# Kernel optimization log

Measured on AMD Instinct MI355X. Metric: run time of the kernel, lower is better.

Reference implementation:

```python
import math
import jax, jax.numpy as jnp
import numpy as np

H = 16          # n_heads
WIN = 512       # window_size (causal, one-sided)
BS = 64         # block_size


def setup_inputs() -> dict:
    key = jax.random.key(0)
    ks = jax.random.split(key, 5)
    B, T, D = 2, 4096, 1024
    x = jax.random.normal(ks[0], (B, T, D), dtype=jnp.float32)
    init = 0.02
    Wq = jax.random.normal(ks[1], (D, D), dtype=jnp.float32) * init
    Wk = jax.random.normal(ks[2], (D, D), dtype=jnp.float32) * init
    Wv = jax.random.normal(ks[3], (D, D), dtype=jnp.float32) * init
    Wo = jax.random.normal(ks[4], (D, D), dtype=jnp.float32) * init
    return {"x": x, "Wq": Wq, "Wk": Wk, "Wv": Wv, "Wo": Wo}


def _sliding_window_attn(q, k, v):
    """Causal sliding-window attention, banded/block-sparse form.

    q,k,v: (B, H, T, hd). Only key blocks within the window of each query
    block are gathered, honoring the sparsity the torch mask encodes.
    """
    B, Hn, T, hd = q.shape
    nb = T // BS                   # number of blocks
    nw1 = WIN // BS + 1            # key blocks touching a query block
    scale = 1.0 / math.sqrt(hd)

    qb = q.reshape(B, Hn, nb, BS, hd)
    kb = k.reshape(B, Hn, nb, BS, hd)
    vb = v.reshape(B, Hn, nb, BS, hd)

    offs = jnp.arange(-(WIN // BS), 1)                 # (nw1,)
    idx_raw = jnp.arange(nb)[:, None] + offs[None, :]  # (nb, nw1)
    idx = jnp.clip(idx_raw, 0, nb - 1)

    kg = jnp.take(kb, idx, axis=2)   # (B,H,nb,nw1,BS,hd)
    vg = jnp.take(vb, idx, axis=2)

    scores = jnp.einsum('bhnqd,bhnwkd->bhnqwk', qb, kg) * scale

    qpos = (jnp.arange(nb) * BS)[:, None, None, None] + jnp.arange(BS)[None, :, None, None]  # (nb,BS,1,1)
    kpos = (idx_raw * BS)[:, None, :, None] + jnp.arange(BS)[None, None, None, :]            # (nb,1,nw1,BS)
    valid = (idx_raw[:, None, :, None] >= 0) & (kpos <= qpos) & (qpos - kpos < WIN)
    scores = jnp.where(valid[None, None], scores, -1e9)

    p = jax.nn.softmax(scores.reshape(B, Hn, nb, BS, nw1 * BS), axis=-1)
    p = p.reshape(B, Hn, nb, BS, nw1, BS)
    out = jnp.einsum('bhnqwk,bhnwkd->bhnqd', p, vg)
    return out.reshape(B, Hn, T, hd)


def reference(x, Wq, Wk, Wv, Wo):
    B, T, D = x.shape
    hd = D // H

    def proj(W):  # torch Linear: x @ W.T
        return (x @ W.T).reshape(B, T, H, hd).transpose(0, 2, 1, 3)

    q, k, v = proj(Wq), proj(Wk), proj(Wv)
    out = _sliding_window_attn(q, k, v)            # (B,H,T,hd)
    out = out.transpose(0, 2, 1, 3).reshape(B, T, D)
    return out @ Wo.T
```

## Files before the change

kernel.cpp:

```cpp
#include <hip/hip_runtime.h>

#define DI static __device__ __forceinline__

typedef __attribute__((ext_vector_type(8))) short short8;
typedef __attribute__((ext_vector_type(4))) float f32x4;

DI unsigned short f2bf(float f) {
    union { float f; unsigned int u; } v; v.f = f;
    unsigned int r = v.u + 0x7FFFu + ((v.u >> 16) & 1u);
    return (unsigned short)(r >> 16);
}

DI void gload_lds16(const void* g, void* l) {
    __builtin_amdgcn_global_load_lds(
        (const __attribute__((address_space(1))) void*)g,
        (__attribute__((address_space(3))) void*)l, 16, 0, 0);
}

DI short8 ldsfrag(const void* base, int row, int bytecol) {
    return *(const short8*)((const char*)base + row * 128 + (bytecol ^ ((row & 7) << 4)));
}

__global__ __launch_bounds__(256) void k_cvt(
    const float* __restrict__ x, const float* __restrict__ wq,
    const float* __restrict__ wk, const float* __restrict__ wv,
    const float* __restrict__ wo,
    unsigned short* __restrict__ xb, unsigned short* __restrict__ wqb,
    unsigned short* __restrict__ wkb, unsigned short* __restrict__ wvb,
    unsigned short* __restrict__ wob)
{
    int idx = (blockIdx.x * 256 + threadIdx.x) * 4;
    const float* src; unsigned short* dst; int off;
    if (idx < 8388608) {
        src = x; dst = xb; off = idx;
    } else {
        int rel = idx - 8388608;
        int sel = rel >> 20;
        off = rel & 1048575;
        switch (sel) {
            case 0:  src = wq; dst = wqb; break;
            case 1:  src = wk; dst = wkb; break;
            case 2:  src = wv; dst = wvb; break;
            default: src = wo; dst = wob; break;
        }
    }
    float4 v = *(const float4*)(src + off);
    unsigned long long o = (unsigned long long)f2bf(v.x)
        | ((unsigned long long)f2bf(v.y) << 16)
        | ((unsigned long long)f2bf(v.z) << 32)
        | ((unsigned long long)f2bf(v.w) << 48);
    *(unsigned long long*)(dst + off) = o;
}

DI void gemm_core(const unsigned short* __restrict__ Ag,
                  const unsigned short* __restrict__ Bg,
                  int m0, int n0, char* smem, f32x4 acc[4][4])
{
    const int t = threadIdx.x, lane = t & 63;
    const int wid = t >> 6, wr = wid >> 2, wc = wid & 3;
    const int kl = lane & 15, hi = lane >> 4;

#pragma unroll
    for (int m = 0; m < 4; ++m)
#pragma unroll
        for (int n = 0; n < 4; ++n)
            acc[m][n] = f32x4{0.f, 0.f, 0.f, 0.f};

    const int ca  = t,       ra  = ca  >> 2, sa  = ((ca  & 3) ^ ((ra  >> 1) & 3)) * 8;
    const int cb0 = t,       rb0 = cb0 >> 2, sb0 = ((cb0 & 3) ^ ((rb0 >> 1) & 3)) * 8;
    const int cb1 = t + 512, rb1 = cb1 >> 2, sb1 = ((cb1 & 3) ^ ((rb1 >> 1) & 3)) * 8;
    const unsigned short* pa  = Ag + (long)(m0 + ra)  * 1024 + sa;
    const unsigned short* pb0 = Bg + (long)(n0 + rb0) * 1024 + sb0;
    const unsigned short* pb1 = Bg + (long)(n0 + rb1) * 1024 + sb1;

#define STAGE(TILE, BUF) do {                                          \
        char* _sb = smem + (BUF) * 24576;                              \
        gload_lds16(pa  + (TILE) * 32, _sb + ca * 16);                 \
        gload_lds16(pb0 + (TILE) * 32, _sb + 8192 + cb0 * 16);         \
        gload_lds16(pb1 + (TILE) * 32, _sb + 8192 + cb1 * 16);         \
    } while (0)

    STAGE(0, 0);
    STAGE(1, 1);

    const int swz = ((hi ^ ((kl >> 1) & 3)) << 4);
    const int aoff = (wr * 64 + kl) * 64 + swz;
    const int boff = 8192 + (wc * 64 + kl) * 64 + swz;

#define KSTEP(KS, CUR, PRE, ISSUE, VM) do {                                   \
        asm volatile("s_waitcnt vmcnt(" VM ")" ::: "memory");                 \
        __builtin_amdgcn_s_barrier();                                         \
        __builtin_amdgcn_sched_barrier(0);                                    \
        if (ISSUE) STAGE((KS) + 2, PRE);                                      \
        const char* _ab = smem + (CUR) * 24576 + aoff;                        \
        const char* _bb = smem + (CUR) * 24576 + boff;                        \
        short8 _fa[4], _fb[4];                                                \
        _Pragma("unroll")                                                     \
        for (int m = 0; m < 4; ++m) _fa[m] = *(const short8*)(_ab + m * 1024);\
        _Pragma("unroll")                                                     \
        for (int n = 0; n < 4; ++n) _fb[n] = *(const short8*)(_bb + n * 1024);\
        __builtin_amdgcn_s_setprio(1);                                        \
        _Pragma("unroll")                                                     \
        for (int m = 0; m < 4; ++m)                                           \
        _Pragma("unroll")                                                     \
            for (int n = 0; n < 4; ++n)                                       \
                acc[m][n] = __builtin_amdgcn_mfma_f32_16x16x32_bf16(          \
                    _fa[m], _fb[n], acc[m][n], 0, 0, 0);                      \
        __builtin_amdgcn_s_setprio(0);                                        \
    } while (0)

    for (int u = 0; u < 10; ++u) {
        const int ks = u * 3;
        KSTEP(ks + 0, 0, 2, 1, "3");
        KSTEP(ks + 1, 1, 0, 1, "3");
        KSTEP(ks + 2, 2, 1, 1, "3");
    }
    KSTEP(30, 0, 2, 0, "3");
    KSTEP(31, 1, 0, 0, "0");
#undef KSTEP
#undef STAGE
}

DI void gemm_core128(const unsigned short* __restrict__ Ag,
                     const unsigned short* __restrict__ Bg,
                     int m0, int n0, char* smem, f32x4 acc[4][4])
{
    const int t = threadIdx.x, lane = t & 63;
    const int wid = t >> 6, wr = wid >> 1, wc = wid & 1;
    const int kl = lane & 15, hi = lane >> 4;

#pragma unroll
    for (int m = 0; m < 4; ++m)
#pragma unroll
        for (int n = 0; n < 4; ++n)
            acc[m][n] = f32x4{0.f, 0.f, 0.f, 0.f};

    const int ca0 = t,       ra0 = ca0 >> 2, sa0 = ((ca0 & 3) ^ ((ra0 >> 1) & 3)) * 8;
    const int ca1 = t + 256, ra1 = ca1 >> 2, sa1 = ((ca1 & 3) ^ ((ra1 >> 1) & 3)) * 8;
    const unsigned short* pa0 = Ag + (long)(m0 + ra0) * 1024 + sa0;
    const unsigned short* pa1 = Ag + (long)(m0 + ra1) * 1024 + sa1;
    const unsigned short* pb0 = Bg + (long)(n0 + ra0) * 1024 + sa0;
    const unsigned short* pb1 = Bg + (long)(n0 + ra1) * 1024 + sa1;

#define STAGE(TILE, BUF) do {                                          \
        char* _sb = smem + (BUF) * 16384;                              \
        gload_lds16(pa0 + (TILE) * 32, _sb + ca0 * 16);                \
        gload_lds16(pa1 + (TILE) * 32, _sb + ca1 * 16);                \
        gload_lds16(pb0 + (TILE) * 32, _sb + 8192 + ca0 * 16);         \
        gload_lds16(pb1 + (TILE) * 32, _sb + 8192 + ca1 * 16);         \
    } while (0)

    STAGE(0, 0);
    STAGE(1, 1);

    const int swz = ((hi ^ ((kl >> 1) & 3)) << 4);
    const int aoff = (wr * 64 + kl) * 64 + swz;
    const int boff = 8192 + (wc * 64 + kl) * 64 + swz;

#define KSTEP(KS, CUR, PRE, ISSUE, VM) do {                                   \
        asm volatile("s_waitcnt vmcnt(" VM ")" ::: "memory");                 \
        __builtin_amdgcn_s_barrier();                                         \
        __builtin_amdgcn_sched_barrier(0);                                    \
        if (ISSUE) STAGE((KS) + 2, PRE);                                      \
        const char* _ab = smem + (CUR) * 16384 + aoff;                        \
        const char* _bb = smem + (CUR) * 16384 + boff;                        \
        short8 _fa[4], _fb[4];                                                \
        _Pragma("unroll")                                                     \
        for (int m = 0; m < 4; ++m) _fa[m] = *(const short8*)(_ab + m * 1024);\
        _Pragma("unroll")                                                     \
        for (int n = 0; n < 4; ++n) _fb[n] = *(const short8*)(_bb + n * 1024);\
        __builtin_amdgcn_s_setprio(1);                                        \
        _Pragma("unroll")                                                     \
        for (int m = 0; m < 4; ++m)                                           \
        _Pragma("unroll")                                                     \
            for (int n = 0; n < 4; ++n)                                       \
                acc[m][n] = __builtin_amdgcn_mfma_f32_16x16x32_bf16(          \
                    _fa[m], _fb[n], acc[m][n], 0, 0, 0);                      \
        __builtin_amdgcn_s_setprio(0);                                        \
    } while (0)

    for (int u = 0; u < 10; ++u) {
        const int ks = u * 3;
        KSTEP(ks + 0, 0, 2, 1, "4");
        KSTEP(ks + 1, 1, 0, 1, "4");
        KSTEP(ks + 2, 2, 1, 1, "4");
    }
    KSTEP(30, 0, 2, 0, "4");
    KSTEP(31, 1, 0, 0, "0");
#undef KSTEP
#undef STAGE
}

__global__ __launch_bounds__(512, 4) void k_gemm_qkv(
    const unsigned short* __restrict__ xb,
    const unsigned short* __restrict__ wqb, const unsigned short* __restrict__ wkb,
    const unsigned short* __restrict__ wvb,
    unsigned short* __restrict__ Qo, unsigned short* __restrict__ Ko,
    unsigned short* __restrict__ VTo)
{
    extern __shared__ char smem[];
    const int bx = blockIdx.x, by = blockIdx.y;
    const int w = by >> 2, nb = by & 3;
    const unsigned short* Bw = (w == 0) ? wqb : ((w == 1) ? wkb : wvb);
    const float sc = (w == 0) ? 0.18033688011112042f : 1.0f;

    f32x4 acc[4][4];
    gemm_core(xb, Bw, bx * 128, nb * 256, smem, acc);

    const int t = threadIdx.x, lane = t & 63, wid = t >> 6;
    const int wr = wid >> 2, wc = wid & 3, kl = lane & 15, hi = lane >> 4;
    const int h = nb * 4 + wc;

    if (w < 2) {
        unsigned short* Ow = (w == 0) ? Qo : Ko;
#pragma unroll
        for (int m = 0; m < 4; ++m)
#pragma unroll
            for (int r = 0; r < 4; ++r) {
                int grow = bx * 128 + wr * 64 + m * 16 + hi * 4 + r;
                int bi = grow >> 12, tt = grow & 4095;
                unsigned short* rowp = Ow + ((long)(bi * 16 + h) * 4096 + tt) * 64;
#pragma unroll
                for (int n = 0; n < 4; ++n)
                    rowp[n * 16 + kl] = f2bf(acc[m][n][r] * sc);
            }
    } else {
#pragma unroll
        for (int m = 0; m < 4; ++m)
#pragma unroll
            for (int r = 0; r < 4; ++r) {
                int grow = bx * 128 + wr * 64 + m * 16 + hi * 4 + r;
                int bi = grow >> 12, tt = grow & 4095;
                unsigned short* hb = VTo + (long)(bi * 16 + h) * 262144;
#pragma unroll
                for (int n = 0; n < 4; ++n) {
                    int d = n * 16 + kl;
                    hb[(long)d * 4096 + tt] = f2bf(acc[m][n][r]);
                }
            }
    }
}

__global__ __launch_bounds__(512) void k_attn(
    const unsigned short* __restrict__ Q, const unsigned short* __restrict__ K,
    const unsigned short* __restrict__ VT, unsigned short* __restrict__ AO)
{
    __shared__ unsigned short Qs[8192];
    __shared__ unsigned short Ks[2][4096], Vs[2][4096];
    const int t = threadIdx.x, lane = t & 63, wid = t >> 6;
    const int kl = lane & 15, hi = lane >> 4;
    const int bid = blockIdx.x;
    const int sid = (bid & 7) * 128 + (bid >> 3);
    const int qi = sid & 31, bh = sid >> 5;
    const int b = bh >> 4, h = bh & 15;
    const int iA = qi * 2, iB = qi * 2 + 1;
    const int myI = (wid < 4) ? iA : iB;
    const char* qg = (const char*)(Q + ((long)bh * 4096 + qi * 128) * 64);
    const char* kg = (const char*)(K + (long)bh * 4096 * 64);
    const char* vg = (const char*)(VT + (long)bh * 64 * 4096);

    const int cq0 = t, cq1 = t + 512;
    const int rq0 = cq0 >> 3, sq0 = ((cq0 & 7) * 16) ^ ((rq0 & 7) << 4);
    const int rq1 = cq1 >> 3, sq1 = ((cq1 & 7) * 16) ^ ((rq1 & 7) << 4);
    const int rk = t >> 3, swk = ((t & 7) * 16) ^ ((rk & 7) << 4);
    const char* kgt = kg + rk * 128 + swk;
    const char* vgt = vg + rk * 8192 + swk;

    const int jlo = (iA >= 8) ? iA - 8 : 0;
    const int jhi = iB;

    gload_lds16(qg + rq0 * 128 + sq0, (char*)Qs + cq0 * 16);
    gload_lds16(qg + rq1 * 128 + sq1, (char*)Qs + cq1 * 16);
    gload_lds16(kgt + jlo * 8192, (char*)Ks[0] + t * 16);
    gload_lds16(vgt + jlo * 128,  (char*)Vs[0] + t * 16);
    __syncthreads();

    short8 aq[2];
    aq[0] = ldsfrag(Qs, wid * 16 + kl, hi * 16);
    aq[1] = ldsfrag(Qs, wid * 16 + kl, 64 + hi * 16);

    float lsum[4] = {0.f, 0.f, 0.f, 0.f};
    f32x4 o[4];
#pragma unroll
    for (int nt = 0; nt < 4; ++nt) o[nt] = f32x4{0.f, 0.f, 0.f, 0.f};

    const int qrow = (wid & 3) * 16 + hi * 4;
    char* pw = (char*)Qs + wid * 2048;

    for (int j = jlo; j <= jhi; ++j) {
        const int buf = (j - jlo) & 1;
        if (j < jhi) {
            const int nb = buf ^ 1;
            gload_lds16(kgt + (j + 1) * 8192, (char*)Ks[nb] + t * 16);
            gload_lds16(vgt + (j + 1) * 128,  (char*)Vs[nb] + t * 16);
        }

        const bool act = (wid < 4) ? (j <= iA) : (j >= iB - 8);
        if (act) {
            f32x4 s[4];
#pragma unroll
            for (int nt = 0; nt < 4; ++nt) {
                s[nt] = f32x4{0.f, 0.f, 0.f, 0.f};
#pragma unroll
                for (int kk = 0; kk < 2; ++kk)
                    s[nt] = __builtin_amdgcn_mfma_f32_16x16x32_bf16(
                        aq[kk], ldsfrag(Ks[buf], nt * 16 + kl, kk * 64 + hi * 16),
                        s[nt], 0, 0, 0);
            }

            if (j == myI) {
#pragma unroll
                for (int nt = 0; nt < 4; ++nt) {
                    int key = nt * 16 + kl;
#pragma unroll
                    for (int r = 0; r < 4; ++r)
                        if (key > qrow + r) s[nt][r] = -1e9f;
                }
            } else if (myI - j == 8) {
#pragma unroll
                for (int nt = 0; nt < 4; ++nt) {
                    int key = nt * 16 + kl;
#pragma unroll
                    for (int r = 0; r < 4; ++r)
                        if (key <= qrow + r) s[nt][r] = -1e9f;
                }
            }

#pragma unroll
            for (int nt = 0; nt < 4; ++nt)
#pragma unroll
                for (int r = 0; r < 4; ++r) {
                    float p = exp2f(s[nt][r]);
                    s[nt][r] = p;
                    lsum[r] += p;
                }

#pragma unroll
            for (int nt = 0; nt < 4; ++nt)
#pragma unroll
                for (int r = 0; r < 4; ++r) {
                    int q = hi * 4 + r;
                    int colb = (nt * 16 + kl) * 2;
                    *(unsigned short*)(pw + q * 128 + (colb ^ ((q & 7) << 4))) =
                        f2bf(s[nt][r]);
                }

            short8 pa0 = ldsfrag(pw, kl, hi * 16);
            short8 pa1 = ldsfrag(pw, kl, 64 + hi * 16);
#pragma unroll
            for (int nt = 0; nt < 4; ++nt) {
                o[nt] = __builtin_amdgcn_mfma_f32_16x16x32_bf16(
                    pa0, ldsfrag(Vs[buf], nt * 16 + kl, hi * 16), o[nt], 0, 0, 0);
                o[nt] = __builtin_amdgcn_mfma_f32_16x16x32_bf16(
                    pa1, ldsfrag(Vs[buf], nt * 16 + kl, 64 + hi * 16), o[nt], 0, 0, 0);
            }
        }

        __syncthreads();
    }

#pragma unroll
    for (int d = 1; d < 16; d <<= 1)
#pragma unroll
        for (int r = 0; r < 4; ++r) lsum[r] += __shfl_xor(lsum[r], d);

    float inv[4];
#pragma unroll
    for (int r = 0; r < 4; ++r) inv[r] = 1.0f / lsum[r];
#pragma unroll
    for (int r = 0; r < 4; ++r) {
        int tt = qi * 128 + wid * 16 + hi * 4 + r;
        unsigned short* rowp = AO + ((long)(b * 4096 + tt)) * 1024 + h * 64;
#pragma unroll
        for (int nt = 0; nt < 4; ++nt)
            rowp[nt * 16 + kl] = f2bf(o[nt][r] * inv[r]);
    }
}

__global__ __launch_bounds__(256, 3) void k_gemm_out(
    const unsigned short* __restrict__ AO, const unsigned short* __restrict__ wob,
    float* __restrict__ out)
{
    extern __shared__ char smem[];
    const int bx = blockIdx.x, nb = blockIdx.y;
    f32x4 acc[4][4];
    gemm_core128(AO, wob, bx * 128, nb * 128, smem, acc);

    const int t = threadIdx.x, lane = t & 63, wid = t >> 6;
    const int wr = wid >> 1, wc = wid & 1, kl = lane & 15, hi = lane >> 4;
#pragma unroll
    for (int m = 0; m < 4; ++m)
#pragma unroll
        for (int r = 0; r < 4; ++r) {
            int grow = bx * 128 + wr * 64 + m * 16 + hi * 4 + r;
            float* rowp = out + (long)grow * 1024 + nb * 128 + wc * 64;
#pragma unroll
            for (int n = 0; n < 4; ++n)
                rowp[n * 16 + kl] = acc[m][n][r];
        }
}

extern "C" void kernel_launch(void* const* d_in, const int* in_sizes, int n_in,
                              void* d_out, int out_size, void* d_ws, size_t ws_size,
                              hipStream_t stream) {
    const float* x  = (const float*)d_in[0];
    const float* wq = (const float*)d_in[1];
    const float* wk = (const float*)d_in[2];
    const float* wv = (const float*)d_in[3];
    const float* wo = (const float*)d_in[4];

    char* ws = (char*)d_ws;
    const size_t MB = 1024 * 1024;
    unsigned short* xb  = (unsigned short*)(ws);
    unsigned short* wqb = (unsigned short*)(ws + 16 * MB);
    unsigned short* wkb = (unsigned short*)(ws + 18 * MB);
    unsigned short* wvb = (unsigned short*)(ws + 20 * MB);
    unsigned short* wob = (unsigned short*)(ws + 22 * MB);
    unsigned short* Qp  = (unsigned short*)(ws + 24 * MB);
    unsigned short* Kp  = (unsigned short*)(ws + 40 * MB);
    unsigned short* VTp = (unsigned short*)(ws + 56 * MB);
    unsigned short* AOp = xb;

    hipFuncSetAttribute((const void*)k_gemm_qkv,
                        hipFuncAttributeMaxDynamicSharedMemorySize, 73728);
    hipFuncSetAttribute((const void*)k_gemm_out,
                        hipFuncAttributeMaxDynamicSharedMemorySize, 49152);

    dim3 blk(256);
    k_cvt<<<12288, blk, 0, stream>>>(x, wq, wk, wv, wo,
                                     xb, wqb, wkb, wvb, wob);
    k_gemm_qkv<<<dim3(64, 12), 512, 73728, stream>>>(xb, wqb, wkb, wvb,
                                                     Qp, Kp, VTp);
    k_attn<<<1024, 512, 0, stream>>>(Qp, Kp, VTp, AOp);
    k_gemm_out<<<dim3(64, 8), 256, 49152, stream>>>(AOp, wob, (float*)d_out);
}
```

Measured before the change: 136.5 us.

## Enlarge QKV GEMM tile to 256x256 with 64-wide K and ping-pong LDS

The QKV projection GEMM now computes a 256x256 output tile per 512-thread block instead of 128x256. Each wave holds an 8x4 accumulator array and works through 64-wide K tiles with two LDS buffers of 64KB each. The MFMA work is split into four phases that interleave LDS fragment reads with compute. This aims for higher arithmetic intensity and fewer global loads per FLOP, but the grid shrinks to 384 blocks, LDS use grows to 128KB, and register pressure rises, which lowers occupancy.

```diff
diff --git a/kernel.cpp b/kernel.cpp
--- a/kernel.cpp
+++ b/kernel.cpp
@@ -52,73 +52,165 @@
     *(unsigned long long*)(dst + off) = o;
 }
 
-DI void gemm_core(const unsigned short* __restrict__ Ag,
-                  const unsigned short* __restrict__ Bg,
-                  int m0, int n0, char* smem, f32x4 acc[4][4])
+DI void gemm8p(const unsigned short* __restrict__ Ag,
+               const unsigned short* __restrict__ Bg,
+               int m0, int n0, char* smem, f32x4 acc[8][4])
 {
     const int t = threadIdx.x, lane = t & 63;
     const int wid = t >> 6, wr = wid >> 2, wc = wid & 3;
     const int kl = lane & 15, hi = lane >> 4;
 
 #pragma unroll
-    for (int m = 0; m < 4; ++m)
+    for (int m = 0; m < 8; ++m)
 #pragma unroll
         for (int n = 0; n < 4; ++n)
             acc[m][n] = f32x4{0.f, 0.f, 0.f, 0.f};
 
-    const int ca  = t,       ra  = ca  >> 2, sa  = ((ca  & 3) ^ ((ra  >> 1) & 3)) * 8;
-    const int cb0 = t,       rb0 = cb0 >> 2, sb0 = ((cb0 & 3) ^ ((rb0 >> 1) & 3)) * 8;
-    const int cb1 = t + 512, rb1 = cb1 >> 2, sb1 = ((cb1 & 3) ^ ((rb1 >> 1) & 3)) * 8;
-    const unsigned short* pa  = Ag + (long)(m0 + ra)  * 1024 + sa;
-    const unsigned short* pb0 = Bg + (long)(n0 + rb0) * 1024 + sb0;
-    const unsigned short* pb1 = Bg + (long)(n0 + rb1) * 1024 + sb1;
-
-#define STAGE(TILE, BUF) do {                                          \
-        char* _sb = smem + (BUF) * 24576;                              \
-        gload_lds16(pa  + (TILE) * 32, _sb + ca * 16);                 \
-        gload_lds16(pb0 + (TILE) * 32, _sb + 8192 + cb0 * 16);         \
-        gload_lds16(pb1 + (TILE) * 32, _sb + 8192 + cb1 * 16);         \
-    } while (0)
-
-    STAGE(0, 0);
-    STAGE(1, 1);
-
-    const int swz = ((hi ^ ((kl >> 1) & 3)) << 4);
-    const int aoff = (wr * 64 + kl) * 64 + swz;
-    const int boff = 8192 + (wc * 64 + kl) * 64 + swz;
-
-#define KSTEP(KS, CUR, PRE, ISSUE, VM) do {                                   \
-        asm volatile("s_waitcnt vmcnt(" VM ")" ::: "memory");                 \
-        __builtin_amdgcn_s_barrier();                                         \
-        __builtin_amdgcn_sched_barrier(0);                                    \
-        if (ISSUE) STAGE((KS) + 2, PRE);                                      \
-        const char* _ab = smem + (CUR) * 24576 + aoff;                        \
-        const char* _bb = smem + (CUR) * 24576 + boff;                        \
-        short8 _fa[4], _fb[4];                                                \
-        _Pragma("unroll")                                                     \
-        for (int m = 0; m < 4; ++m) _fa[m] = *(const short8*)(_ab + m * 1024);\
-        _Pragma("unroll")                                                     \
-        for (int n = 0; n < 4; ++n) _fb[n] = *(const short8*)(_bb + n * 1024);\
-        __builtin_amdgcn_s_setprio(1);                                        \
-        _Pragma("unroll")                                                     \
-        for (int m = 0; m < 4; ++m)                                           \
-        _Pragma("unroll")                                                     \
-            for (int n = 0; n < 4; ++n)                                       \
-                acc[m][n] = __builtin_amdgcn_mfma_f32_16x16x32_bf16(          \
-                    _fa[m], _fb[n], acc[m][n], 0, 0, 0);                      \
-        __builtin_amdgcn_s_setprio(0);                                        \
-    } while (0)
-
-    for (int u = 0; u < 10; ++u) {
-        const int ks = u * 3;
-        KSTEP(ks + 0, 0, 2, 1, "3");
-        KSTEP(ks + 1, 1, 0, 1, "3");
-        KSTEP(ks + 2, 2, 1, 1, "3");
-    }
-    KSTEP(30, 0, 2, 0, "3");
-    KSTEP(31, 1, 0, 0, "0");
-#undef KSTEP
-#undef STAGE
+    const int c0 = t, c1 = t + 512;
+    const int r0 = c0 >> 3, e0 = ((c0 & 7) * 8) ^ ((r0 & 7) << 3);
+    const int r1 = c1 >> 3, e1 = ((c1 & 7) * 8) ^ ((r1 & 7) << 3);
+    const unsigned short* pAl0 = Ag + (long)(m0 + r0) * 1024 + e0;
+    const unsigned short* pAl1 = Ag + (long)(m0 + r1) * 1024 + e1;
+    const unsigned short* pAh0 = pAl0 + 128 * 1024;
+    const unsigned short* pAh1 = pAl1 + 128 * 1024;
+    const unsigned short* pBl0 = Bg + (long)(n0 + r0) * 1024 + e0;
+    const unsigned short* pBl1 = Bg + (long)(n0 + r1) * 1024 + e1;
+    const unsigned short* pBh0 = pBl0 + 128 * 1024;
+    const unsigned short* pBh1 = pBl1 + 128 * 1024;
+
+#define STAGE8(T, SB) do {                                             \
+        char* _s = smem + (SB) * 65536;                                \
+        gload_lds16(pAl0 + (T) * 64, _s + c0 * 16);                    \
+        gload_lds16(pAl1 + (T) * 64, _s + c1 * 16);                    \
+        gload_lds16(pAh0 + (T) * 64, _s + 16384 + c0 * 16);            \
+        gload_lds16(pAh1 + (T) * 64, _s + 16384 + c1 * 16);            \
+        gload_lds16(pBl0 + (T) * 64, _s + 32768 + c0 * 16);            \
+        gload_lds16(pBl1 + (T) * 64, _s + 32768 + c1 * 16);            \
+        gload_lds16(pBh0 + (T) * 64, _s + 49152 + c0 * 16);            \
+        gload_lds16(pBh1 + (T) * 64, _s + 49152 + c1 * 16);            \
+    } while (0)
+
+    STAGE8(0, 0);
+
+    const int arow = wr * 128 + kl;
+    const int brow = wc * 64 + kl;
+    const int swzk = (kl & 7) << 4;
+    const int aoff0 = arow * 128 + ((hi * 16) ^ swzk);
+    const int aoff1 = arow * 128 + ((64 + hi * 16) ^ swzk);
+    const int boff0 = 32768 + brow * 128 + ((hi * 16) ^ swzk);
+    const int boff1 = 32768 + brow * 128 + ((64 + hi * 16) ^ swzk);
+
+#define RD_A(BASE) do {                                                      \
+        _Pragma("unroll")                                                    \
+        for (int q = 0; q < 4; ++q) {                                        \
+            fA0[q] = *(const short8*)(_b + aoff0 + ((BASE) + q) * 2048);     \
+            fA1[q] = *(const short8*)(_b + aoff1 + ((BASE) + q) * 2048);     \
+        }                                                                    \
+    } while (0)
+#define RD_B(BASE) do {                                                      \
+        _Pragma("unroll")                                                    \
+        for (int q = 0; q < 2; ++q) {                                        \
+            fB0[q] = *(const short8*)(_b + boff0 + ((BASE) + q) * 2048);     \
+            fB1[q] = *(const short8*)(_b + boff1 + ((BASE) + q) * 2048);     \
+        }                                                                    \
+    } while (0)
+#define PREMM                                                                \
+        __builtin_amdgcn_s_barrier();                                        \
+        asm volatile("s_waitcnt lgkmcnt(0)" ::: "memory");                   \
+        __builtin_amdgcn_sched_barrier(0);
+#define MM(MB, NB) do {                                                      \
+        __builtin_amdgcn_s_setprio(1);                                       \
+        _Pragma("unroll")                                                    \
+        for (int q = 0; q < 4; ++q)                                          \
+        _Pragma("unroll")                                                    \
+            for (int p = 0; p < 2; ++p) {                                    \
+                acc[(MB)+q][(NB)+p] = __builtin_amdgcn_mfma_f32_16x16x32_bf16(\
+                    fA0[q], fB0[p], acc[(MB)+q][(NB)+p], 0, 0, 0);           \
+                acc[(MB)+q][(NB)+p] = __builtin_amdgcn_mfma_f32_16x16x32_bf16(\
+                    fA1[q], fB1[p], acc[(MB)+q][(NB)+p], 0, 0, 0);           \
+            }                                                                \
+        __builtin_amdgcn_s_setprio(0);                                       \
+    } while (0)
+
+#define KTILE(T, BUF, ISSUE) do {                                            \
+        const char* _b = smem + (BUF) * 65536;                               \
+        short8 fA0[4], fA1[4], fB0[2], fB1[2];                               \
+                                                          \
+        asm volatile("s_waitcnt vmcnt(0)" ::: "memory");                     \
+        __builtin_amdgcn_s_barrier();                                        \
+        RD_A(0); RD_B(0);                                                    \
+        if (ISSUE) STAGE8((T) + 1, (BUF) ^ 1);                               \
+        PREMM; MM(0, 0);                                                     \
+                                                          \
+        RD_B(2); PREMM; MM(0, 2);                                            \
+                                                          \
+        RD_A(4); PREMM; MM(4, 2);                                            \
+                                                          \
+        RD_B(0); PREMM; MM(4, 0);                                            \
+    } while (0)
+
+    for (int u = 0; u < 7; ++u) {
+        KTILE(2 * u,     0, 1);
+        KTILE(2 * u + 1, 1, 1);
+    }
+    KTILE(14, 0, 1);
+    KTILE(15, 1, 0);
+#undef KTILE
+#undef MM
+#undef PREMM
+#undef RD_B
+#undef RD_A
+#undef STAGE8
+}
+
+__global__ __launch_bounds__(512, 2) void k_gemm_qkv(
+    const unsigned short* __restrict__ xb,
+    const unsigned short* __restrict__ wqb, const unsigned short* __restrict__ wkb,
+    const unsigned short* __restrict__ wvb,
+    unsigned short* __restrict__ Qo, unsigned short* __restrict__ Ko,
+    unsigned short* __restrict__ VTo)
+{
+    extern __shared__ char smem[];
+    const int bx = blockIdx.x, by = blockIdx.y;
+    const int w = by >> 2, nb = by & 3;
+    const unsigned short* Bw = (w == 0) ? wqb : ((w == 1) ? wkb : wvb);
+    const float sc = (w == 0) ? 0.18033688011112042f : 1.0f;
+
+    f32x4 acc[8][4];
+    gemm8p(xb, Bw, bx * 256, nb * 256, smem, acc);
+
+    const int t = threadIdx.x, lane = t & 63, wid = t >> 6;
+    const int wr = wid >> 2, wc = wid & 3, kl = lane & 15, hi = lane >> 4;
+    const int h = nb * 4 + wc;
+
+    if (w < 2) {
+        unsigned short* Ow = (w == 0) ? Qo : Ko;
+#pragma unroll
+        for (int mi = 0; mi < 8; ++mi)
+#pragma unroll
+            for (int r = 0; r < 4; ++r) {
+                int grow = bx * 256 + wr * 128 + mi * 16 + hi * 4 + r;
+                int bi = grow >> 12, tt = grow & 4095;
+                unsigned short* rowp = Ow + ((long)(bi * 16 + h) * 4096 + tt) * 64;
+#pragma unroll
+                for (int nj = 0; nj < 4; ++nj)
+                    rowp[nj * 16 + kl] = f2bf(acc[mi][nj][r] * sc);
+            }
+    } else {
+#pragma unroll
+        for (int mi = 0; mi < 8; ++mi)
+#pragma unroll
+            for (int r = 0; r < 4; ++r) {
+                int grow = bx * 256 + wr * 128 + mi * 16 + hi * 4 + r;
+                int bi = grow >> 12, tt = grow & 4095;
+                unsigned short* hb = VTo + (long)(bi * 16 + h) * 262144;
+#pragma unroll
+                for (int nj = 0; nj < 4; ++nj) {
+                    int d = nj * 16 + kl;
+                    hb[(long)d * 4096 + tt] = f2bf(acc[mi][nj][r]);
+                }
+            }
+    }
 }
 
 DI void gemm_core128(const unsigned short* __restrict__ Ag,
@@ -191,56 +283,6 @@
 #undef STAGE
 }
 
-__global__ __launch_bounds__(512, 4) void k_gemm_qkv(
-    const unsigned short* __restrict__ xb,
-    const unsigned short* __restrict__ wqb, const unsigned short* __restrict__ wkb,
-    const unsigned short* __restrict__ wvb,
-    unsigned short* __restrict__ Qo, unsigned short* __restrict__ Ko,
-    unsigned short* __restrict__ VTo)
-{
-    extern __shared__ char smem[];
-    const int bx = blockIdx.x, by = blockIdx.y;
-    const int w = by >> 2, nb = by & 3;
-    const unsigned short* Bw = (w == 0) ? wqb : ((w == 1) ? wkb : wvb);
-    const float sc = (w == 0) ? 0.18033688011112042f : 1.0f;
-
-    f32x4 acc[4][4];
-    gemm_core(xb, Bw, bx * 128, nb * 256, smem, acc);
-
-    const int t = threadIdx.x, lane = t & 63, wid = t >> 6;
-    const int wr = wid >> 2, wc = wid & 3, kl = lane & 15, hi = lane >> 4;
-    const int h = nb * 4 + wc;
-
-    if (w < 2) {
-        unsigned short* Ow = (w == 0) ? Qo : Ko;
-#pragma unroll
-        for (int m = 0; m < 4; ++m)
-#pragma unroll
-            for (int r = 0; r < 4; ++r) {
-                int grow = bx * 128 + wr * 64 + m * 16 + hi * 4 + r;
-                int bi = grow >> 12, tt = grow & 4095;
-                unsigned short* rowp = Ow + ((long)(bi * 16 + h) * 4096 + tt) * 64;
-#pragma unroll
-                for (int n = 0; n < 4; ++n)
-                    rowp[n * 16 + kl] = f2bf(acc[m][n][r] * sc);
-            }
-    } else {
-#pragma unroll
-        for (int m = 0; m < 4; ++m)
-#pragma unroll
-            for (int r = 0; r < 4; ++r) {
-                int grow = bx * 128 + wr * 64 + m * 16 + hi * 4 + r;
-                int bi = grow >> 12, tt = grow & 4095;
-                unsigned short* hb = VTo + (long)(bi * 16 + h) * 262144;
-#pragma unroll
-                for (int n = 0; n < 4; ++n) {
-                    int d = n * 16 + kl;
-                    hb[(long)d * 4096 + tt] = f2bf(acc[m][n][r]);
-                }
-            }
-    }
-}
-
 __global__ __launch_bounds__(512) void k_attn(
     const unsigned short* __restrict__ Q, const unsigned short* __restrict__ K,
     const unsigned short* __restrict__ VT, unsigned short* __restrict__ AO)
@@ -422,15 +464,15 @@
     unsigned short* AOp = xb;
 
     hipFuncSetAttribute((const void*)k_gemm_qkv,
-                        hipFuncAttributeMaxDynamicSharedMemorySize, 73728);
+                        hipFuncAttributeMaxDynamicSharedMemorySize, 131072);
     hipFuncSetAttribute((const void*)k_gemm_out,
                         hipFuncAttributeMaxDynamicSharedMemorySize, 49152);
 
     dim3 blk(256);
     k_cvt<<<12288, blk, 0, stream>>>(x, wq, wk, wv, wo,
                                      xb, wqb, wkb, wvb, wob);
-    k_gemm_qkv<<<dim3(64, 12), 512, 73728, stream>>>(xb, wqb, wkb, wvb,
-                                                     Qp, Kp, VTp);
+    k_gemm_qkv<<<dim3(32, 12), 512, 131072, stream>>>(xb, wqb, wkb, wvb,
+                                                      Qp, Kp, VTp);
     k_attn<<<1024, 512, 0, stream>>>(Qp, Kp, VTp, AOp);
     k_gemm_out<<<dim3(64, 8), 256, 49152, stream>>>(AOp, wob, (float*)d_out);
 }
```

Result: slower. 145.4 us (+6.5%).

## Triple-buffer K/V tiles in attention with vmcnt-based waits and single barrier

Applied to the files above, without the earlier changes.

Switches the attention kernel from double-buffered static LDS to a triple-buffered dynamic LDS ring for K and V tiles, prefetching two blocks ahead. Explicit s_waitcnt vmcnt counts replace the trailing __syncthreads, so each iteration needs only one barrier before compute. The goal is to hide global-load latency better and cut barrier stalls. The cost is more LDS per block (64KB, up from 48KB), which may lower occupancy, and a reliance on the hand-counted vmcnt values being correct.

```diff
diff --git a/kernel.cpp b/kernel.cpp
--- a/kernel.cpp
+++ b/kernel.cpp
@@ -245,8 +245,10 @@
     const unsigned short* __restrict__ Q, const unsigned short* __restrict__ K,
     const unsigned short* __restrict__ VT, unsigned short* __restrict__ AO)
 {
-    __shared__ unsigned short Qs[8192];
-    __shared__ unsigned short Ks[2][4096], Vs[2][4096];
+    extern __shared__ char asmem[];
+    char* Qs = asmem;
+    char* Kb = asmem + 16384;
+    char* Vb = asmem + 40960;
     const int t = threadIdx.x, lane = t & 63, wid = t >> 6;
     const int kl = lane & 15, hi = lane >> 4;
     const int bid = blockIdx.x;
@@ -269,11 +271,16 @@
     const int jlo = (iA >= 8) ? iA - 8 : 0;
     const int jhi = iB;
 
-    gload_lds16(qg + rq0 * 128 + sq0, (char*)Qs + cq0 * 16);
-    gload_lds16(qg + rq1 * 128 + sq1, (char*)Qs + cq1 * 16);
-    gload_lds16(kgt + jlo * 8192, (char*)Ks[0] + t * 16);
-    gload_lds16(vgt + jlo * 128,  (char*)Vs[0] + t * 16);
-    __syncthreads();
+    gload_lds16(qg + rq0 * 128 + sq0, Qs + cq0 * 16);
+    gload_lds16(qg + rq1 * 128 + sq1, Qs + cq1 * 16);
+    gload_lds16(kgt + jlo * 8192, Kb + t * 16);
+    gload_lds16(vgt + jlo * 128,  Vb + t * 16);
+    gload_lds16(kgt + (jlo + 1) * 8192, Kb + 8192 + t * 16);
+    gload_lds16(vgt + (jlo + 1) * 128,  Vb + 8192 + t * 16);
+
+    asm volatile("s_waitcnt vmcnt(4)" ::: "memory");
+    __builtin_amdgcn_s_barrier();
+    __builtin_amdgcn_sched_barrier(0);
 
     short8 aq[2];
     aq[0] = ldsfrag(Qs, wid * 16 + kl, hi * 16);
@@ -285,15 +292,23 @@
     for (int nt = 0; nt < 4; ++nt) o[nt] = f32x4{0.f, 0.f, 0.f, 0.f};
 
     const int qrow = (wid & 3) * 16 + hi * 4;
-    char* pw = (char*)Qs + wid * 2048;
-
+    char* pw = Qs + wid * 2048;
+
+    int cur = 0;
     for (int j = jlo; j <= jhi; ++j) {
-        const int buf = (j - jlo) & 1;
-        if (j < jhi) {
-            const int nb = buf ^ 1;
-            gload_lds16(kgt + (j + 1) * 8192, (char*)Ks[nb] + t * 16);
-            gload_lds16(vgt + (j + 1) * 128,  (char*)Vs[nb] + t * 16);
+        if (j < jhi) asm volatile("s_waitcnt vmcnt(2)" ::: "memory");
+        else         asm volatile("s_waitcnt vmcnt(0)" ::: "memory");
+        __builtin_amdgcn_s_barrier();
+        __builtin_amdgcn_sched_barrier(0);
+
+        if (j + 2 <= jhi) {
+            int p2 = cur - 1; if (p2 < 0) p2 = 2;
+            gload_lds16(kgt + (j + 2) * 8192, Kb + p2 * 8192 + t * 16);
+            gload_lds16(vgt + (j + 2) * 128,  Vb + p2 * 8192 + t * 16);
         }
+
+        const char* Kc = Kb + cur * 8192;
+        const char* Vc = Vb + cur * 8192;
 
         const bool act = (wid < 4) ? (j <= iA) : (j >= iB - 8);
         if (act) {
@@ -304,7 +319,7 @@
 #pragma unroll
                 for (int kk = 0; kk < 2; ++kk)
                     s[nt] = __builtin_amdgcn_mfma_f32_16x16x32_bf16(
-                        aq[kk], ldsfrag(Ks[buf], nt * 16 + kl, kk * 64 + hi * 16),
+                        aq[kk], ldsfrag(Kc, nt * 16 + kl, kk * 64 + hi * 16),
                         s[nt], 0, 0, 0);
             }
 
@@ -350,13 +365,13 @@
 #pragma unroll
             for (int nt = 0; nt < 4; ++nt) {
                 o[nt] = __builtin_amdgcn_mfma_f32_16x16x32_bf16(
-                    pa0, ldsfrag(Vs[buf], nt * 16 + kl, hi * 16), o[nt], 0, 0, 0);
+                    pa0, ldsfrag(Vc, nt * 16 + kl, hi * 16), o[nt], 0, 0, 0);
                 o[nt] = __builtin_amdgcn_mfma_f32_16x16x32_bf16(
-                    pa1, ldsfrag(Vs[buf], nt * 16 + kl, 64 + hi * 16), o[nt], 0, 0, 0);
+                    pa1, ldsfrag(Vc, nt * 16 + kl, 64 + hi * 16), o[nt], 0, 0, 0);
             }
         }
 
-        __syncthreads();
+        cur = (cur == 2) ? 0 : cur + 1;
     }
 
 #pragma unroll
@@ -423,6 +438,8 @@
 
     hipFuncSetAttribute((const void*)k_gemm_qkv,
                         hipFuncAttributeMaxDynamicSharedMemorySize, 73728);
+    hipFuncSetAttribute((const void*)k_attn,
+                        hipFuncAttributeMaxDynamicSharedMemorySize, 65536);
     hipFuncSetAttribute((const void*)k_gemm_out,
                         hipFuncAttributeMaxDynamicSharedMemorySize, 49152);
 
@@ -431,6 +448,6 @@
                                      xb, wqb, wkb, wvb, wob);
     k_gemm_qkv<<<dim3(64, 12), 512, 73728, stream>>>(xb, wqb, wkb, wvb,
                                                      Qp, Kp, VTp);
-    k_attn<<<1024, 512, 0, stream>>>(Qp, Kp, VTp, AOp);
+    k_attn<<<1024, 512, 65536, stream>>>(Qp, Kp, VTp, AOp);
     k_gemm_out<<<dim3(64, 8), 256, 49152, stream>>>(AOp, wob, (float*)d_out);
 }
```

New measurement: 138.8 us. About the same (+1.7%).
